# Kernel tuning notes

Measured on AMD Instinct MI355X. Metric: run time of the kernel, lower is better.

Reference implementation:

```python
import jax, jax.numpy as jnp
import numpy as np

C_M = 256
C_Z = 128
S = 256   # number of MSA sequences (global `s` in source)
R = 384   # number of residues (global `r` in source)
C = 32    # per-head channel dim
H = 8     # N_head
EPS = 1e-5


def _layer_norm(x, w, b):
    mu = jnp.mean(x, axis=-1, keepdims=True)
    var = jnp.mean(jnp.square(x - mu), axis=-1, keepdims=True)
    return (x - mu) * jax.lax.rsqrt(var + EPS) * w + b


def setup_inputs() -> dict:
    key = jax.random.key(0)
    ks = jax.random.split(key, 8)
    w = 0.02
    return {
        "msa": jax.random.normal(ks[0], (S, R, C_M), dtype=jnp.float32),
        "pair": jax.random.normal(ks[1], (R, R, C_Z), dtype=jnp.float32),
        "norm_msa_w": jnp.ones((H, C_M), jnp.float32),
        "norm_msa_b": jnp.zeros((H, C_M), jnp.float32),
        "wq": jax.random.normal(ks[2], (H, C, C_M), dtype=jnp.float32) * w,
        "wk": jax.random.normal(ks[3], (H, C, C_M), dtype=jnp.float32) * w,
        "wv": jax.random.normal(ks[4], (H, C, C_M), dtype=jnp.float32) * w,
        "norm_pair_w": jnp.ones((H, C_Z), jnp.float32),
        "norm_pair_b": jnp.zeros((H, C_Z), jnp.float32),
        "wb": jax.random.normal(ks[5], (H, S, C_Z), dtype=jnp.float32) * w,
        "wg": jax.random.normal(ks[6], (H, C, C_M), dtype=jnp.float32) * w,
        "out_w": jax.random.normal(ks[7], (C_M, C * H), dtype=jnp.float32) * w,
        "out_b": jnp.zeros((C_M,), jnp.float32),
    }


def reference(msa, pair, norm_msa_w, norm_msa_b, wq, wk, wv,
              norm_pair_w, norm_pair_b, wb, wg, out_w, out_b):
    inv_sqrt_c = 1.0 / np.sqrt(C).astype(np.float32)
    pair_flat = pair.reshape(-1, C_Z)  # (R*R, C_Z); view(-1, c_z)
    outs = []
    for i in range(H):
        # NOTE: faithful to source — msa is OVERWRITTEN by the per-head norm,
        # so normalization compounds across the head loop.
        msa = _layer_norm(msa, norm_msa_w[i], norm_msa_b[i])
        q = jnp.einsum('src,dc->srd', msa, wq[i])  # (S,R,C)
        k = jnp.einsum('src,dc->srd', msa, wk[i])
        v = jnp.einsum('src,dc->srd', msa, wv[i])
        # pair bias: LN -> Linear(c_z -> s) -> reshape (not transpose!) to (S,R,R)
        b = jnp.einsum('pc,sc->ps', _layer_norm(pair_flat, norm_pair_w[i], norm_pair_b[i]), wb[i])
        b = b.reshape(S, R, R)
        g = jax.nn.sigmoid(jnp.einsum('src,dc->srd', msa, wg[i]))  # (S,R,C)
        logits = inv_sqrt_c * (jnp.einsum('src,stc->srt', q, k) + b)  # (S,R,R)
        a = jax.nn.softmax(logits, axis=-2)  # softmax over QUERY axis, as in source
        o = g * jnp.einsum('srt,stc->src', a, v)  # (S,R,C)
        outs.append(o)
    out = jnp.concatenate(outs, axis=2)  # (S,R,C*H)
    return jnp.einsum('srk,mk->srm', out, out_w) + out_b  # (S,R,C_M)
```

## Files before the change

### kernel.cpp

```cpp
#include <hip/hip_runtime.h>

typedef unsigned short bf16_t;
typedef uint4  __attribute__((may_alias)) uint4_a;
typedef uint2  __attribute__((may_alias)) uint2_a;
typedef float4 __attribute__((may_alias)) float4_a;
typedef short bf16x8 __attribute__((ext_vector_type(8)));
typedef bf16x8 __attribute__((may_alias)) bf16x8_a;
typedef float f32x4 __attribute__((ext_vector_type(4)));

#define MFMA16(a, b, c) __builtin_amdgcn_mfma_f32_16x16x32_bf16((a), (b), (c), 0, 0, 0)

constexpr int kS  = 256;
constexpr int kR  = 384;
constexpr int kCM = 256;
constexpr int kCZ = 128;
constexpr int kC  = 32;
constexpr int kH  = 8;
constexpr int kP  = kR * kR;
constexpr int kM  = kS * kR;

#define EPSF 1e-5f
#define SCALEF 0.17677669529663687f

__device__ __forceinline__ float bf2f(bf16_t u) {
  return __uint_as_float(((unsigned int)u) << 16);
}
__device__ __forceinline__ bf16_t f2bf(float f) {
  unsigned int u = __float_as_uint(f);
  u += 0x7fffu + ((u >> 16) & 1u);
  return (bf16_t)(u >> 16);
}

__global__ __launch_bounds__(256) void k_pair_fused(const float* __restrict__ pair,
                                                    bf16_t* __restrict__ pair_bf,
                                                    float* __restrict__ mu,
                                                    float* __restrict__ rstd) {
  int row = blockIdx.x * 8 + (threadIdx.x >> 5);
  int l = threadIdx.x & 31;
  const float* src = pair + (size_t)row * kCZ + l * 4;
  float4_a x = *(const float4_a*)src;
  float s1 = x.x + x.y + x.z + x.w;
  float s2 = x.x * x.x + x.y * x.y + x.z * x.z + x.w * x.w;
#pragma unroll
  for (int off = 16; off > 0; off >>= 1) {
    s1 += __shfl_xor(s1, off);
    s2 += __shfl_xor(s2, off);
  }
  float m = s1 * (1.0f / kCZ);
  float v = s2 * (1.0f / kCZ) - m * m;
  float rs = rsqrtf(fmaxf(v, 0.0f) + EPSF);
  if (l == 0) {
    mu[row] = m;
    rstd[row] = rs;
  }
  uint2 u;
  u.x = (unsigned)f2bf(x.x) | ((unsigned)f2bf(x.y) << 16);
  u.y = (unsigned)f2bf(x.z) | ((unsigned)f2bf(x.w) << 16);
  *(uint2_a*)(pair_bf + (size_t)row * kCZ + l * 4) = u;
}

__global__ __launch_bounds__(256) void k_msa_ln(const float* __restrict__ src_f,
                                                const bf16_t* __restrict__ src_b,
                                                bf16_t* __restrict__ dst,
                                                const float* __restrict__ wall,
                                                const float* __restrict__ ball,
                                                int head, int first) {
  int row = blockIdx.x * 8 + (threadIdx.x >> 5);
  int l = threadIdx.x & 31;
  int c0 = l * 8;
  float x[8];
  if (first) {
    float4_a a = *(const float4_a*)(src_f + (size_t)row * kCM + c0);
    float4_a b = *(const float4_a*)(src_f + (size_t)row * kCM + c0 + 4);
    x[0] = a.x; x[1] = a.y; x[2] = a.z; x[3] = a.w;
    x[4] = b.x; x[5] = b.y; x[6] = b.z; x[7] = b.w;
  } else {
    union { bf16x8 v; bf16_t h[8]; } uu;
    uu.v = *(const bf16x8_a*)(src_b + (size_t)row * kCM + c0);
#pragma unroll
    for (int j = 0; j < 8; ++j) x[j] = bf2f(uu.h[j]);
  }
  float s1 = 0.f, s2 = 0.f;
#pragma unroll
  for (int j = 0; j < 8; ++j) {
    s1 += x[j];
    s2 += x[j] * x[j];
  }
#pragma unroll
  for (int off = 16; off > 0; off >>= 1) {
    s1 += __shfl_xor(s1, off);
    s2 += __shfl_xor(s2, off);
  }
  float m = s1 * (1.0f / kCM);
  float var = s2 * (1.0f / kCM) - m * m;
  float rs = rsqrtf(fmaxf(var, 0.0f) + EPSF);
  float4_a wa = *(const float4_a*)(wall + head * kCM + c0);
  float4_a wb4 = *(const float4_a*)(wall + head * kCM + c0 + 4);
  float4_a ba = *(const float4_a*)(ball + head * kCM + c0);
  float4_a bb4 = *(const float4_a*)(ball + head * kCM + c0 + 4);
  float wv[8] = {wa.x, wa.y, wa.z, wa.w, wb4.x, wb4.y, wb4.z, wb4.w};
  float bv[8] = {ba.x, ba.y, ba.z, ba.w, bb4.x, bb4.y, bb4.z, bb4.w};
  bf16_t h[8];
#pragma unroll
  for (int j = 0; j < 8; ++j) h[j] = f2bf((x[j] - m) * rs * wv[j] + bv[j]);
  uint4 u;
  u.x = (unsigned)h[0] | ((unsigned)h[1] << 16);
  u.y = (unsigned)h[2] | ((unsigned)h[3] << 16);
  u.z = (unsigned)h[4] | ((unsigned)h[5] << 16);
  u.w = (unsigned)h[6] | ((unsigned)h[7] << 16);
  *(uint4_a*)(dst + (size_t)row * kCM + c0) = u;
}

__global__ __launch_bounds__(256) void k_pack_wcat_all(const float* __restrict__ wq,
                                                       const float* __restrict__ wk,
                                                       const float* __restrict__ wv,
                                                       const float* __restrict__ wg,
                                                       bf16_t* __restrict__ Wcat) {
  int gid = blockIdx.x * 256 + threadIdx.x;
  int head = gid >> 15;
  int idx = gid & 32767;
  int j = idx >> 8;
  int c = idx & 255;
  const float* src = (j < 32) ? wq : (j < 64) ? wk : (j < 96) ? wv : wg;
  int d = j & 31;
  Wcat[gid] = f2bf(src[(head * kC + d) * kCM + c]);
}

__global__ __launch_bounds__(256) void k_pack_bias_all(const float* __restrict__ wb,
                                                       const float* __restrict__ npw,
                                                       const float* __restrict__ npb,
                                                       bf16_t* __restrict__ wbeff,
                                                       float* __restrict__ beta,
                                                       float* __restrict__ sw) {
  int head = blockIdx.x;
  int j = threadIdx.x;
  float sb = 0.f, ssw = 0.f;
  for (int c = 0; c < kCZ; ++c) {
    float w = wb[(head * kS + j) * kCZ + c];
    float e = w * npw[head * kCZ + c];
    wbeff[(size_t)head * kS * kCZ + j * kCZ + c] = f2bf(e);
    ssw += e;
    sb += w * npb[head * kCZ + c];
  }
  sw[head * kS + j] = ssw;
  beta[head * kS + j] = sb;
}

__global__ __launch_bounds__(256) void k_pack_outw(const float* __restrict__ in,
                                                   bf16_t* __restrict__ out) {
  int i = blockIdx.x * 256 + threadIdx.x;
  out[i] = f2bf(in[i]);
}

__global__ __launch_bounds__(256) void k_gemm_qkvg_mx(const bf16_t* __restrict__ A,
                                                      const bf16_t* __restrict__ B,
                                                      bf16_t* __restrict__ q,
                                                      bf16_t* __restrict__ k,
                                                      bf16_t* __restrict__ v,
                                                      bf16_t* __restrict__ g) {
  __shared__ bf16_t As[128 * 32];
  __shared__ bf16_t Bs[128 * 32];
  int m0 = blockIdx.x * 128;
  int tid = threadIdx.x;
  int w = tid >> 6, L = tid & 63, l15 = L & 15, q4 = L >> 4;
  int wm = w >> 1, wn = w & 1;
  f32x4 acc[4][4] = {};
  for (int k0 = 0; k0 < 256; k0 += 32) {
#pragma unroll
    for (int rep = 0; rep < 2; ++rep) {
      int idx = tid + rep * 256;
      int row = idx >> 2, sg = idx & 3;
      *(uint4_a*)&As[row * 32 + sg * 8] = *(const uint4_a*)(A + (size_t)(m0 + row) * 256 + k0 + sg * 8);
      *(uint4_a*)&Bs[row * 32 + sg * 8] = *(const uint4_a*)(B + (size_t)row * 256 + k0 + sg * 8);
    }
    __syncthreads();
    bf16x8 af[4], bfr[4];
#pragma unroll
    for (int mt = 0; mt < 4; ++mt) af[mt] = *(const bf16x8_a*)&As[(wm * 64 + mt * 16 + l15) * 32 + q4 * 8];
#pragma unroll
    for (int nt = 0; nt < 4; ++nt) bfr[nt] = *(const bf16x8_a*)&Bs[(wn * 64 + nt * 16 + l15) * 32 + q4 * 8];
#pragma unroll
    for (int mt = 0; mt < 4; ++mt)
#pragma unroll
      for (int nt = 0; nt < 4; ++nt) acc[mt][nt] = MFMA16(af[mt], bfr[nt], acc[mt][nt]);
    __syncthreads();
  }
#pragma unroll
  for (int mt = 0; mt < 4; ++mt)
#pragma unroll
    for (int nt = 0; nt < 4; ++nt) {
      int n = wn * 64 + nt * 16 + l15;
      int mat = n >> 5, d = n & 31;
      bf16_t* tgt = (mat == 0) ? q : (mat == 1) ? k : (mat == 2) ? v : g;
#pragma unroll
      for (int i = 0; i < 4; ++i) {
        int m = m0 + wm * 64 + mt * 16 + q4 * 4 + i;
        float val = acc[mt][nt][i];
        if (mat == 3) val = 1.0f / (1.0f + __expf(-val));
        tgt[(size_t)m * kC + d] = f2bf(val);
      }
    }
}

__global__ __launch_bounds__(256) void k_gemm_bias_mx(const bf16_t* __restrict__ A,
                                                      const bf16_t* __restrict__ B,
                                                      const float* __restrict__ mu,
                                                      const float* __restrict__ rstd,
                                                      const float* __restrict__ sw,
                                                      const float* __restrict__ beta,
                                                      bf16_t* __restrict__ Bm) {
  __shared__ bf16_t As[128 * 32];
  __shared__ bf16_t Bs[128 * 32];
  int m0 = blockIdx.x * 128;
  int n0 = blockIdx.y * 128;
  int tid = threadIdx.x;
  int w = tid >> 6, L = tid & 63, l15 = L & 15, q4 = L >> 4;
  int wm = w >> 1, wn = w & 1;
  f32x4 acc[4][4] = {};
  for (int k0 = 0; k0 < 128; k0 += 32) {
#pragma unroll
    for (int rep = 0; rep < 2; ++rep) {
      int idx = tid + rep * 256;
      int row = idx >> 2, sg = idx & 3;
      *(uint4_a*)&As[row * 32 + sg * 8] = *(const uint4_a*)(A + (size_t)(m0 + row) * 128 + k0 + sg * 8);
      *(uint4_a*)&Bs[row * 32 + sg * 8] = *(const uint4_a*)(B + (size_t)(n0 + row) * 128 + k0 + sg * 8);
    }
    __syncthreads();
    bf16x8 af[4], bfr[4];
#pragma unroll
    for (int mt = 0; mt < 4; ++mt) af[mt] = *(const bf16x8_a*)&As[(wm * 64 + mt * 16 + l15) * 32 + q4 * 8];
#pragma unroll
    for (int nt = 0; nt < 4; ++nt) bfr[nt] = *(const bf16x8_a*)&Bs[(wn * 64 + nt * 16 + l15) * 32 + q4 * 8];
#pragma unroll
    for (int mt = 0; mt < 4; ++mt)
#pragma unroll
      for (int nt = 0; nt < 4; ++nt) acc[mt][nt] = MFMA16(af[mt], bfr[nt], acc[mt][nt]);
    __syncthreads();
  }
#pragma unroll
  for (int mt = 0; mt < 4; ++mt)
#pragma unroll
    for (int i = 0; i < 4; ++i) {
      int m = m0 + wm * 64 + mt * 16 + q4 * 4 + i;
      float mp = mu[m], rp = rstd[m];
#pragma unroll
      for (int nt = 0; nt < 4; ++nt) {
        int n = n0 + wn * 64 + nt * 16 + l15;
        float val = rp * (acc[mt][nt][i] - mp * sw[n]) + beta[n];
        Bm[(size_t)m * kS + n] = f2bf(val);
      }
    }
}

__global__ __launch_bounds__(256) void k_logits(const bf16_t* __restrict__ q,
                                                const bf16_t* __restrict__ kmat,
                                                bf16_t* __restrict__ Bm) {
  int s = blockIdx.y;
  int t0 = blockIdx.x * 64;
  int tid = threadIdx.x;
  int w = tid >> 6, L = tid & 63, l15 = L & 15, q4 = L >> 4;
  __shared__ float red[4][64];
  __shared__ float msh[64], dish[64];
  bf16_t* bmS = Bm + (size_t)s * kP;
  f32x4 acc[6][4];
#pragma unroll
  for (int rt = 0; rt < 6; ++rt)
#pragma unroll
    for (int nt = 0; nt < 4; ++nt)
#pragma unroll
      for (int i = 0; i < 4; ++i) {
        int r = w * 96 + rt * 16 + q4 * 4 + i;
        int t = t0 + nt * 16 + l15;
        acc[rt][nt][i] = bf2f(bmS[(size_t)r * kR + t]);
      }
  const bf16_t* qs = q + (size_t)s * kR * kC;
  const bf16_t* ks = kmat + (size_t)s * kR * kC;
  bf16x8 bfr[4];
#pragma unroll
  for (int nt = 0; nt < 4; ++nt)
    bfr[nt] = *(const bf16x8_a*)(ks + (size_t)(t0 + nt * 16 + l15) * kC + q4 * 8);
#pragma unroll
  for (int rt = 0; rt < 6; ++rt) {
    bf16x8 af = *(const bf16x8_a*)(qs + (size_t)(w * 96 + rt * 16 + l15) * kC + q4 * 8);
#pragma unroll
    for (int nt = 0; nt < 4; ++nt) acc[rt][nt] = MFMA16(af, bfr[nt], acc[rt][nt]);
  }
#pragma unroll
  for (int rt = 0; rt < 6; ++rt)
#pragma unroll
    for (int nt = 0; nt < 4; ++nt) acc[rt][nt] *= SCALEF;
  float mx[4] = {-3.0e38f, -3.0e38f, -3.0e38f, -3.0e38f};
#pragma unroll
  for (int rt = 0; rt < 6; ++rt)
#pragma unroll
    for (int nt = 0; nt < 4; ++nt)
#pragma unroll
      for (int i = 0; i < 4; ++i) mx[nt] = fmaxf(mx[nt], acc[rt][nt][i]);
#pragma unroll
  for (int nt = 0; nt < 4; ++nt) {
    mx[nt] = fmaxf(mx[nt], __shfl_xor(mx[nt], 16));
    mx[nt] = fmaxf(mx[nt], __shfl_xor(mx[nt], 32));
  }
  if (L < 16) {
#pragma unroll
    for (int nt = 0; nt < 4; ++nt) red[w][nt * 16 + L] = mx[nt];
  }
  __syncthreads();
  if (tid < 64) {
    float m = fmaxf(fmaxf(red[0][tid], red[1][tid]), fmaxf(red[2][tid], red[3][tid]));
    msh[tid] = m;
  }
  __syncthreads();
  float mt_[4];
#pragma unroll
  for (int nt = 0; nt < 4; ++nt) mt_[nt] = msh[nt * 16 + l15];
  float sm[4] = {0.f, 0.f, 0.f, 0.f};
#pragma unroll
  for (int rt = 0; rt < 6; ++rt)
#pragma unroll
    for (int nt = 0; nt < 4; ++nt)
#pragma unroll
      for (int i = 0; i < 4; ++i) {
        float e = __expf(acc[rt][nt][i] - mt_[nt]);
        acc[rt][nt][i] = e;
        sm[nt] += e;
      }
#pragma unroll
  for (int nt = 0; nt < 4; ++nt) {
    sm[nt] += __shfl_xor(sm[nt], 16);
    sm[nt] += __shfl_xor(sm[nt], 32);
  }
  __syncthreads();
  if (L < 16) {
#pragma unroll
    for (int nt = 0; nt < 4; ++nt) red[w][nt * 16 + L] = sm[nt];
  }
  __syncthreads();
  if (tid < 64) {
    float d = red[0][tid] + red[1][tid] + red[2][tid] + red[3][tid];
    dish[tid] = 1.0f / d;
  }
  __syncthreads();
  float di[4];
#pragma unroll
  for (int nt = 0; nt < 4; ++nt) di[nt] = dish[nt * 16 + l15];
#pragma unroll
  for (int rt = 0; rt < 6; ++rt)
#pragma unroll
    for (int nt = 0; nt < 4; ++nt)
#pragma unroll
      for (int i = 0; i < 4; ++i) {
        int r = w * 96 + rt * 16 + q4 * 4 + i;
        int t = t0 + nt * 16 + l15;
        bmS[(size_t)r * kR + t] = f2bf(acc[rt][nt][i] * di[nt]);
      }
}

__global__ __launch_bounds__(256) void k_pv(const bf16_t* __restrict__ Am,
                                            const bf16_t* __restrict__ v,
                                            const bf16_t* __restrict__ g,
                                            float* __restrict__ o, int head) {
  int s = blockIdx.y;
  int r0 = blockIdx.x * 64;
  int tid = threadIdx.x;
  int w = tid >> 6, L = tid & 63, l15 = L & 15, q4 = L >> 4;
  __shared__ bf16_t vT[32 * 392];
#pragma unroll
  for (int rep = 0; rep < 6; ++rep) {
    int idx = tid + rep * 256;
    int t = idx >> 2, sg = idx & 3;
    union { uint4 u; bf16_t h[8]; } uu;
    uu.u = *(const uint4_a*)(v + (size_t)(s * kR + t) * kC + sg * 8);
#pragma unroll
    for (int j = 0; j < 8; ++j) vT[(sg * 8 + j) * 392 + t] = uu.h[j];
  }
  __syncthreads();
  const bf16_t* aS = Am + (size_t)s * kP + (size_t)(r0 + 16 * w + l15) * kR;
  f32x4 acc[2] = {};
#pragma unroll
  for (int kk = 0; kk < 12; ++kk) {
    bf16x8 af = *(const bf16x8_a*)(aS + kk * 32 + q4 * 8);
#pragma unroll
    for (int nt = 0; nt < 2; ++nt) {
      bf16x8 bfv = *(const bf16x8_a*)&vT[(nt * 16 + l15) * 392 + kk * 32 + q4 * 8];
      acc[nt] = MFMA16(af, bfv, acc[nt]);
    }
  }
#pragma unroll
  for (int nt = 0; nt < 2; ++nt)
#pragma unroll
    for (int i = 0; i < 4; ++i) {
      int r = r0 + 16 * w + q4 * 4 + i;
      int c = nt * 16 + l15;
      float val = acc[nt][i] * bf2f(g[(size_t)(s * kR + r) * kC + c]);
      o[(size_t)(s * kR + r) * kCM + head * kC + c] = val;
    }
}

__global__ __launch_bounds__(256) void k_gemm_final_mx(const float* __restrict__ OA,
                                                       const bf16_t* __restrict__ Bw,
                                                       const float* __restrict__ bias,
                                                       float* __restrict__ out) {
  __shared__ bf16_t As[2 * 64 * 32];
  __shared__ bf16_t Bs[256 * 32];
  int m0 = blockIdx.x * 64;
  int tid = threadIdx.x;
  int w = tid >> 6, L = tid & 63, l15 = L & 15, q4 = L >> 4;
  f32x4 acc[4][4] = {};
  for (int kc = 0; kc < 256; kc += 32) {
    {
      int row = tid >> 2, sg = tid & 3;
      const float* src = OA + (size_t)(m0 + row) * kCM + kc + sg * 8;
      float4_a f0 = *(const float4_a*)src;
      float4_a f1 = *(const float4_a*)(src + 4);
      float ff[8] = {f0.x, f0.y, f0.z, f0.w, f1.x, f1.y, f1.z, f1.w};
      uint4 uh, ul;
      bf16_t hi[8], lo[8];
#pragma unroll
      for (int j = 0; j < 8; ++j) {
        hi[j] = f2bf(ff[j]);
        lo[j] = f2bf(ff[j] - bf2f(hi[j]));
      }
      uh.x = (unsigned)hi[0] | ((unsigned)hi[1] << 16); uh.y = (unsigned)hi[2] | ((unsigned)hi[3] << 16);
      uh.z = (unsigned)hi[4] | ((unsigned)hi[5] << 16); uh.w = (unsigned)hi[6] | ((unsigned)hi[7] << 16);
      ul.x = (unsigned)lo[0] | ((unsigned)lo[1] << 16); ul.y = (unsigned)lo[2] | ((unsigned)lo[3] << 16);
      ul.z = (unsigned)lo[4] | ((unsigned)lo[5] << 16); ul.w = (unsigned)lo[6] | ((unsigned)lo[7] << 16);
      *(uint4_a*)&As[row * 32 + sg * 8] = uh;
      *(uint4_a*)&As[2048 + row * 32 + sg * 8] = ul;
    }
#pragma unroll
    for (int rep = 0; rep < 4; ++rep) {
      int idx = tid + rep * 256;
      int row = idx >> 2, sg = idx & 3;
      *(uint4_a*)&Bs[row * 32 + sg * 8] = *(const uint4_a*)(Bw + (size_t)row * kCM + kc + sg * 8);
    }
    __syncthreads();
    bf16x8 bfr[4];
#pragma unroll
    for (int nt = 0; nt < 4; ++nt) bfr[nt] = *(const bf16x8_a*)&Bs[(w * 64 + nt * 16 + l15) * 32 + q4 * 8];
#pragma unroll
    for (int half = 0; half < 2; ++half)
#pragma unroll
      for (int mt = 0; mt < 4; ++mt) {
        bf16x8 af = *(const bf16x8_a*)&As[half * 2048 + (mt * 16 + l15) * 32 + q4 * 8];
#pragma unroll
        for (int nt = 0; nt < 4; ++nt) acc[mt][nt] = MFMA16(af, bfr[nt], acc[mt][nt]);
      }
    __syncthreads();
  }
#pragma unroll
  for (int mt = 0; mt < 4; ++mt)
#pragma unroll
    for (int nt = 0; nt < 4; ++nt) {
      int n = w * 64 + nt * 16 + l15;
      float bn = bias[n];
#pragma unroll
      for (int i = 0; i < 4; ++i) {
        int m = m0 + mt * 16 + q4 * 4 + i;
        out[(size_t)m * kCM + n] = acc[mt][nt][i] + bn;
      }
    }
}

extern "C" void kernel_launch(void* const* d_in, const int* in_sizes, int n_in,
                              void* d_out, int out_size, void* d_ws, size_t ws_size,
                              hipStream_t stream) {
  (void)in_sizes; (void)n_in; (void)out_size; (void)ws_size;
  const float* msa_in = (const float*)d_in[0];
  const float* pair   = (const float*)d_in[1];
  const float* nmw    = (const float*)d_in[2];
  const float* nmb    = (const float*)d_in[3];
  const float* wq     = (const float*)d_in[4];
  const float* wk     = (const float*)d_in[5];
  const float* wv     = (const float*)d_in[6];
  const float* npw    = (const float*)d_in[7];
  const float* npb    = (const float*)d_in[8];
  const float* wb     = (const float*)d_in[9];
  const float* wg     = (const float*)d_in[10];
  const float* outw   = (const float*)d_in[11];
  const float* outb   = (const float*)d_in[12];
  float* out = (float*)d_out;

  char* ws = (char*)d_ws;
  size_t off = 0;
  bf16_t* msa_cur  = (bf16_t*)(ws + off); off += (size_t)kM * kCM * 2;
  bf16_t* pair_bf  = (bf16_t*)(ws + off); off += (size_t)kP * kCZ * 2;
  bf16_t* Bm       = (bf16_t*)(ws + off); off += (size_t)kP * kS * 2;
  bf16_t* qb       = (bf16_t*)(ws + off); off += (size_t)kM * kC * 2;
  bf16_t* kb       = (bf16_t*)(ws + off); off += (size_t)kM * kC * 2;
  bf16_t* vb       = (bf16_t*)(ws + off); off += (size_t)kM * kC * 2;
  bf16_t* gb       = (bf16_t*)(ws + off); off += (size_t)kM * kC * 2;
  float* mu_p      = (float*)(ws + off);  off += (size_t)kP * 4;
  float* rstd_p    = (float*)(ws + off);  off += (size_t)kP * 4;
  bf16_t* Wcat_all = (bf16_t*)(ws + off); off += (size_t)kH * 128 * 256 * 2;
  bf16_t* wbef_all = (bf16_t*)(ws + off); off += (size_t)kH * 256 * 128 * 2;
  bf16_t* outw_bf  = (bf16_t*)(ws + off); off += (size_t)256 * 256 * 2;
  float* beta_all  = (float*)(ws + off);  off += (size_t)kH * 256 * 4;
  float* sw_all    = (float*)(ws + off);  off += (size_t)kH * 256 * 4;

  k_pair_fused<<<kP / 8, 256, 0, stream>>>(pair, pair_bf, mu_p, rstd_p);
  k_pack_outw<<<256, 256, 0, stream>>>(outw, outw_bf);
  k_pack_wcat_all<<<kH * 128, 256, 0, stream>>>(wq, wk, wv, wg, Wcat_all);
  k_pack_bias_all<<<kH, 256, 0, stream>>>(wb, npw, npb, wbef_all, beta_all, sw_all);

  for (int h = 0; h < kH; ++h) {
    k_msa_ln<<<kM / 8, 256, 0, stream>>>(msa_in, msa_cur, msa_cur, nmw, nmb, h, h == 0 ? 1 : 0);
    k_gemm_qkvg_mx<<<kM / 128, 256, 0, stream>>>(msa_cur, Wcat_all + (size_t)h * 128 * 256,
                                                 qb, kb, vb, gb);
    k_gemm_bias_mx<<<dim3(kP / 128, 2), 256, 0, stream>>>(pair_bf, wbef_all + (size_t)h * 256 * 128,
                                                          mu_p, rstd_p,
                                                          sw_all + h * 256, beta_all + h * 256, Bm);
    k_logits<<<dim3(6, kS), 256, 0, stream>>>(qb, kb, Bm);
    k_pv<<<dim3(6, kS), 256, 0, stream>>>(Bm, vb, gb, out, h);
  }

  k_gemm_final_mx<<<kM / 64, 256, 0, stream>>>(out, outw_bf, outb, out);
}
```

Measured before the change: 1.513 ms.

## Fuse logits, softmax and PV into one attention kernel per head

After: 1.325 ms. 12.5% less time.

```diff
diff --git a/kernel.cpp b/kernel.cpp
--- a/kernel.cpp
+++ b/kernel.cpp
@@ -137,13 +137,13 @@
   float sb = 0.f, ssw = 0.f;
   for (int c = 0; c < kCZ; ++c) {
     float w = wb[(head * kS + j) * kCZ + c];
-    float e = w * npw[head * kCZ + c];
+    float e = w * npw[head * kCZ + c] * SCALEF;
     wbeff[(size_t)head * kS * kCZ + j * kCZ + c] = f2bf(e);
     ssw += e;
     sb += w * npb[head * kCZ + c];
   }
   sw[head * kS + j] = ssw;
-  beta[head * kS + j] = sb;
+  beta[head * kS + j] = sb * SCALEF;
 }
 
 __global__ __launch_bounds__(256) void k_pack_outw(const float* __restrict__ in,
@@ -157,7 +157,8 @@
                                                       bf16_t* __restrict__ q,
                                                       bf16_t* __restrict__ k,
                                                       bf16_t* __restrict__ v,
-                                                      bf16_t* __restrict__ g) {
+                                                      bf16_t* __restrict__ g_all,
+                                                      int head) {
   __shared__ bf16_t As[128 * 32];
   __shared__ bf16_t Bs[128 * 32];
   int m0 = blockIdx.x * 128;
@@ -191,13 +192,20 @@
     for (int nt = 0; nt < 4; ++nt) {
       int n = wn * 64 + nt * 16 + l15;
       int mat = n >> 5, d = n & 31;
-      bf16_t* tgt = (mat == 0) ? q : (mat == 1) ? k : (mat == 2) ? v : g;
 #pragma unroll
       for (int i = 0; i < 4; ++i) {
         int m = m0 + wm * 64 + mt * 16 + q4 * 4 + i;
         float val = acc[mt][nt][i];
-        if (mat == 3) val = 1.0f / (1.0f + __expf(-val));
-        tgt[(size_t)m * kC + d] = f2bf(val);
+        if (mat == 0) {
+          q[(size_t)m * kC + d] = f2bf(val * SCALEF);
+        } else if (mat == 1) {
+          k[(size_t)m * kC + d] = f2bf(val);
+        } else if (mat == 2) {
+          v[(size_t)m * kC + d] = f2bf(val);
+        } else {
+          float sg = 1.0f / (1.0f + __expf(-val));
+          g_all[(size_t)m * kCM + head * kC + d] = f2bf(sg);
+        }
       }
     }
 }
@@ -252,152 +260,132 @@
     }
 }
 
-__global__ __launch_bounds__(256) void k_logits(const bf16_t* __restrict__ q,
-                                                const bf16_t* __restrict__ kmat,
-                                                bf16_t* __restrict__ Bm) {
-  int s = blockIdx.y;
-  int t0 = blockIdx.x * 64;
+__global__ __launch_bounds__(256, 1) void k_attn(const bf16_t* __restrict__ q,
+                                                 const bf16_t* __restrict__ kmat,
+                                                 const bf16_t* __restrict__ v,
+                                                 const bf16_t* __restrict__ Bm,
+                                                 float* __restrict__ o0,
+                                                 float* __restrict__ o1,
+                                                 int head) {
+  int tb = blockIdx.x;
+  int s  = blockIdx.y;
   int tid = threadIdx.x;
   int w = tid >> 6, L = tid & 63, l15 = L & 15, q4 = L >> 4;
-  __shared__ float red[4][64];
-  __shared__ float msh[64], dish[64];
-  bf16_t* bmS = Bm + (size_t)s * kP;
-  f32x4 acc[6][4];
-#pragma unroll
-  for (int rt = 0; rt < 6; ++rt)
-#pragma unroll
-    for (int nt = 0; nt < 4; ++nt)
-#pragma unroll
-      for (int i = 0; i < 4; ++i) {
-        int r = w * 96 + rt * 16 + q4 * 4 + i;
-        int t = t0 + nt * 16 + l15;
-        acc[rt][nt][i] = bf2f(bmS[(size_t)r * kR + t]);
-      }
-  const bf16_t* qs = q + (size_t)s * kR * kC;
-  const bf16_t* ks = kmat + (size_t)s * kR * kC;
-  bf16x8 bfr[4];
-#pragma unroll
-  for (int nt = 0; nt < 4; ++nt)
-    bfr[nt] = *(const bf16x8_a*)(ks + (size_t)(t0 + nt * 16 + l15) * kC + q4 * 8);
-#pragma unroll
-  for (int rt = 0; rt < 6; ++rt) {
-    bf16x8 af = *(const bf16x8_a*)(qs + (size_t)(w * 96 + rt * 16 + l15) * kC + q4 * 8);
-#pragma unroll
-    for (int nt = 0; nt < 4; ++nt) acc[rt][nt] = MFMA16(af, bfr[nt], acc[rt][nt]);
-  }
-#pragma unroll
-  for (int rt = 0; rt < 6; ++rt)
-#pragma unroll
-    for (int nt = 0; nt < 4; ++nt) acc[rt][nt] *= SCALEF;
-  float mx[4] = {-3.0e38f, -3.0e38f, -3.0e38f, -3.0e38f};
-#pragma unroll
-  for (int rt = 0; rt < 6; ++rt)
-#pragma unroll
-    for (int nt = 0; nt < 4; ++nt)
-#pragma unroll
-      for (int i = 0; i < 4; ++i) mx[nt] = fmaxf(mx[nt], acc[rt][nt][i]);
-#pragma unroll
-  for (int nt = 0; nt < 4; ++nt) {
-    mx[nt] = fmaxf(mx[nt], __shfl_xor(mx[nt], 16));
-    mx[nt] = fmaxf(mx[nt], __shfl_xor(mx[nt], 32));
-  }
-  if (L < 16) {
-#pragma unroll
-    for (int nt = 0; nt < 4; ++nt) red[w][nt * 16 + L] = mx[nt];
-  }
-  __syncthreads();
-  if (tid < 64) {
-    float m = fmaxf(fmaxf(red[0][tid], red[1][tid]), fmaxf(red[2][tid], red[3][tid]));
-    msh[tid] = m;
-  }
-  __syncthreads();
-  float mt_[4];
-#pragma unroll
-  for (int nt = 0; nt < 4; ++nt) mt_[nt] = msh[nt * 16 + l15];
-  float sm[4] = {0.f, 0.f, 0.f, 0.f};
-#pragma unroll
-  for (int rt = 0; rt < 6; ++rt)
-#pragma unroll
-    for (int nt = 0; nt < 4; ++nt)
-#pragma unroll
-      for (int i = 0; i < 4; ++i) {
-        float e = __expf(acc[rt][nt][i] - mt_[nt]);
-        acc[rt][nt][i] = e;
-        sm[nt] += e;
-      }
-#pragma unroll
-  for (int nt = 0; nt < 4; ++nt) {
-    sm[nt] += __shfl_xor(sm[nt], 16);
-    sm[nt] += __shfl_xor(sm[nt], 32);
-  }
-  __syncthreads();
-  if (L < 16) {
-#pragma unroll
-    for (int nt = 0; nt < 4; ++nt) red[w][nt * 16 + L] = sm[nt];
-  }
-  __syncthreads();
-  if (tid < 64) {
-    float d = red[0][tid] + red[1][tid] + red[2][tid] + red[3][tid];
-    dish[tid] = 1.0f / d;
-  }
-  __syncthreads();
-  float di[4];
-#pragma unroll
-  for (int nt = 0; nt < 4; ++nt) di[nt] = dish[nt * 16 + l15];
-#pragma unroll
-  for (int rt = 0; rt < 6; ++rt)
-#pragma unroll
-    for (int nt = 0; nt < 4; ++nt)
-#pragma unroll
-      for (int i = 0; i < 4; ++i) {
-        int r = w * 96 + rt * 16 + q4 * 4 + i;
-        int t = t0 + nt * 16 + l15;
-        bmS[(size_t)r * kR + t] = f2bf(acc[rt][nt][i] * di[nt]);
-      }
-}
-
-__global__ __launch_bounds__(256) void k_pv(const bf16_t* __restrict__ Am,
-                                            const bf16_t* __restrict__ v,
-                                            const bf16_t* __restrict__ g,
-                                            float* __restrict__ o, int head) {
-  int s = blockIdx.y;
-  int r0 = blockIdx.x * 64;
-  int tid = threadIdx.x;
-  int w = tid >> 6, L = tid & 63, l15 = L & 15, q4 = L >> 4;
-  __shared__ bf16_t vT[32 * 392];
-#pragma unroll
-  for (int rep = 0; rep < 6; ++rep) {
+  float* opart = tb ? o1 : o0;
+  __shared__ bf16_t vT[32 * 200];
+  __shared__ bf16_t Psh[64 * 192];
+
+  int tbase = tb * 192;
+#pragma unroll
+  for (int rep = 0; rep < 3; ++rep) {
     int idx = tid + rep * 256;
     int t = idx >> 2, sg = idx & 3;
     union { uint4 u; bf16_t h[8]; } uu;
-    uu.u = *(const uint4_a*)(v + (size_t)(s * kR + t) * kC + sg * 8);
-#pragma unroll
-    for (int j = 0; j < 8; ++j) vT[(sg * 8 + j) * 392 + t] = uu.h[j];
+    uu.u = *(const uint4_a*)(v + (size_t)(s * kR + tbase + t) * kC + sg * 8);
+#pragma unroll
+    for (int j = 0; j < 8; ++j) vT[(sg * 8 + j) * 200 + t] = uu.h[j];
   }
   __syncthreads();
-  const bf16_t* aS = Am + (size_t)s * kP + (size_t)(r0 + 16 * w + l15) * kR;
-  f32x4 acc[2] = {};
-#pragma unroll
-  for (int kk = 0; kk < 12; ++kk) {
-    bf16x8 af = *(const bf16x8_a*)(aS + kk * 32 + q4 * 8);
-#pragma unroll
-    for (int nt = 0; nt < 2; ++nt) {
-      bf16x8 bfv = *(const bf16x8_a*)&vT[(nt * 16 + l15) * 392 + kk * 32 + q4 * 8];
-      acc[nt] = MFMA16(af, bfv, acc[nt]);
-    }
-  }
-#pragma unroll
-  for (int nt = 0; nt < 2; ++nt)
-#pragma unroll
-    for (int i = 0; i < 4; ++i) {
-      int r = r0 + 16 * w + q4 * 4 + i;
-      int c = nt * 16 + l15;
-      float val = acc[nt][i] * bf2f(g[(size_t)(s * kR + r) * kC + c]);
-      o[(size_t)(s * kR + r) * kCM + head * kC + c] = val;
-    }
-}
-
-__global__ __launch_bounds__(256) void k_gemm_final_mx(const float* __restrict__ OA,
+  bf16x8 bfv[12];
+#pragma unroll
+  for (int kk = 0; kk < 6; ++kk)
+#pragma unroll
+    for (int ct = 0; ct < 2; ++ct)
+      bfv[kk * 2 + ct] = *(const bf16x8_a*)&vT[(ct * 16 + l15) * 200 + kk * 32 + q4 * 8];
+
+  int t0 = tbase + 48 * w;
+  const bf16_t* bmS = Bm + (size_t)s * kP;
+  f32x4 acc[24][3];
+#pragma unroll
+  for (int rt = 0; rt < 24; ++rt)
+#pragma unroll
+    for (int tt = 0; tt < 3; ++tt)
+#pragma unroll
+      for (int i = 0; i < 4; ++i)
+        acc[rt][tt][i] = bf2f(bmS[(size_t)(rt * 16 + q4 * 4 + i) * kR + t0 + tt * 16 + l15]);
+
+  const bf16_t* qs = q + (size_t)s * kR * kC;
+  const bf16_t* kp = kmat + (size_t)s * kR * kC;
+  bf16x8 bk[3];
+#pragma unroll
+  for (int tt = 0; tt < 3; ++tt)
+    bk[tt] = *(const bf16x8_a*)(kp + (size_t)(t0 + tt * 16 + l15) * kC + q4 * 8);
+#pragma unroll
+  for (int rt = 0; rt < 24; ++rt) {
+    bf16x8 af = *(const bf16x8_a*)(qs + (size_t)(rt * 16 + l15) * kC + q4 * 8);
+#pragma unroll
+    for (int tt = 0; tt < 3; ++tt) acc[rt][tt] = MFMA16(af, bk[tt], acc[rt][tt]);
+  }
+
+  float mx[3] = {-3.0e38f, -3.0e38f, -3.0e38f};
+#pragma unroll
+  for (int rt = 0; rt < 24; ++rt)
+#pragma unroll
+    for (int tt = 0; tt < 3; ++tt)
+#pragma unroll
+      for (int i = 0; i < 4; ++i) mx[tt] = fmaxf(mx[tt], acc[rt][tt][i]);
+#pragma unroll
+  for (int tt = 0; tt < 3; ++tt) {
+    mx[tt] = fmaxf(mx[tt], __shfl_xor(mx[tt], 16));
+    mx[tt] = fmaxf(mx[tt], __shfl_xor(mx[tt], 32));
+  }
+  float sm[3] = {0.f, 0.f, 0.f};
+#pragma unroll
+  for (int rt = 0; rt < 24; ++rt)
+#pragma unroll
+    for (int tt = 0; tt < 3; ++tt)
+#pragma unroll
+      for (int i = 0; i < 4; ++i) {
+        float e = __expf(acc[rt][tt][i] - mx[tt]);
+        acc[rt][tt][i] = e;
+        sm[tt] += e;
+      }
+#pragma unroll
+  for (int tt = 0; tt < 3; ++tt) {
+    sm[tt] += __shfl_xor(sm[tt], 16);
+    sm[tt] += __shfl_xor(sm[tt], 32);
+  }
+  float di[3];
+#pragma unroll
+  for (int tt = 0; tt < 3; ++tt) di[tt] = 1.0f / sm[tt];
+
+#pragma unroll
+  for (int c = 0; c < 6; ++c) {
+#pragma unroll
+    for (int j = 0; j < 4; ++j)
+#pragma unroll
+      for (int tt = 0; tt < 3; ++tt)
+#pragma unroll
+        for (int i = 0; i < 4; ++i) {
+          int rl = j * 16 + q4 * 4 + i;
+          int tl = 48 * w + tt * 16 + l15;
+          Psh[rl * 192 + (tl ^ ((rl & 7) << 3))] = f2bf(acc[4 * c + j][tt][i] * di[tt]);
+        }
+    __syncthreads();
+    f32x4 pacc[2] = {};
+    int rr = w * 16 + l15;
+#pragma unroll
+    for (int kk = 0; kk < 6; ++kk) {
+      int e = kk * 32 + q4 * 8;
+      bf16x8 af = *(const bf16x8_a*)&Psh[rr * 192 + (e ^ ((rr & 7) << 3))];
+#pragma unroll
+      for (int ct = 0; ct < 2; ++ct) pacc[ct] = MFMA16(af, bfv[kk * 2 + ct], pacc[ct]);
+    }
+#pragma unroll
+    for (int ct = 0; ct < 2; ++ct)
+#pragma unroll
+      for (int i = 0; i < 4; ++i) {
+        int r = c * 64 + w * 16 + q4 * 4 + i;
+        int cc = ct * 16 + l15;
+        opart[(size_t)(s * kR + r) * kCM + head * kC + cc] = pacc[ct][i];
+      }
+    __syncthreads();
+  }
+}
+
+__global__ __launch_bounds__(256) void k_gemm_final_mx(const float* __restrict__ pA,
+                                                       const float* __restrict__ pB,
+                                                       const bf16_t* __restrict__ gall,
                                                        const bf16_t* __restrict__ Bw,
                                                        const float* __restrict__ bias,
                                                        float* __restrict__ out) {
@@ -410,10 +398,17 @@
   for (int kc = 0; kc < 256; kc += 32) {
     {
       int row = tid >> 2, sg = tid & 3;
-      const float* src = OA + (size_t)(m0 + row) * kCM + kc + sg * 8;
-      float4_a f0 = *(const float4_a*)src;
-      float4_a f1 = *(const float4_a*)(src + 4);
-      float ff[8] = {f0.x, f0.y, f0.z, f0.w, f1.x, f1.y, f1.z, f1.w};
+      size_t base = (size_t)(m0 + row) * kCM + kc + sg * 8;
+      float4_a a0 = *(const float4_a*)(pA + base);
+      float4_a a1 = *(const float4_a*)(pA + base + 4);
+      float4_a b0 = *(const float4_a*)(pB + base);
+      float4_a b1 = *(const float4_a*)(pB + base + 4);
+      union { bf16x8 v; bf16_t h[8]; } gg;
+      gg.v = *(const bf16x8_a*)(gall + base);
+      float ff[8] = {a0.x + b0.x, a0.y + b0.y, a0.z + b0.z, a0.w + b0.w,
+                     a1.x + b1.x, a1.y + b1.y, a1.z + b1.z, a1.w + b1.w};
+#pragma unroll
+      for (int j = 0; j < 8; ++j) ff[j] *= bf2f(gg.h[j]);
       uint4 uh, ul;
       bf16_t hi[8], lo[8];
 #pragma unroll
@@ -489,7 +484,8 @@
   bf16_t* qb       = (bf16_t*)(ws + off); off += (size_t)kM * kC * 2;
   bf16_t* kb       = (bf16_t*)(ws + off); off += (size_t)kM * kC * 2;
   bf16_t* vb       = (bf16_t*)(ws + off); off += (size_t)kM * kC * 2;
-  bf16_t* gb       = (bf16_t*)(ws + off); off += (size_t)kM * kC * 2;
+  bf16_t* g_all    = (bf16_t*)(ws + off); off += (size_t)kM * kCM * 2;
+  float*  pB       = (float*)(ws + off);  off += (size_t)kM * kCM * 4;
   float* mu_p      = (float*)(ws + off);  off += (size_t)kP * 4;
   float* rstd_p    = (float*)(ws + off);  off += (size_t)kP * 4;
   bf16_t* Wcat_all = (bf16_t*)(ws + off); off += (size_t)kH * 128 * 256 * 2;
@@ -506,13 +502,12 @@
   for (int h = 0; h < kH; ++h) {
     k_msa_ln<<<kM / 8, 256, 0, stream>>>(msa_in, msa_cur, msa_cur, nmw, nmb, h, h == 0 ? 1 : 0);
     k_gemm_qkvg_mx<<<kM / 128, 256, 0, stream>>>(msa_cur, Wcat_all + (size_t)h * 128 * 256,
-                                                 qb, kb, vb, gb);
+                                                 qb, kb, vb, g_all, h);
     k_gemm_bias_mx<<<dim3(kP / 128, 2), 256, 0, stream>>>(pair_bf, wbef_all + (size_t)h * 256 * 128,
                                                           mu_p, rstd_p,
                                                           sw_all + h * 256, beta_all + h * 256, Bm);
-    k_logits<<<dim3(6, kS), 256, 0, stream>>>(qb, kb, Bm);
-    k_pv<<<dim3(6, kS), 256, 0, stream>>>(Bm, vb, gb, out, h);
-  }
-
-  k_gemm_final_mx<<<kM / 64, 256, 0, stream>>>(out, outw_bf, outb, out);
-}
+    k_attn<<<dim3(2, kS), 256, 0, stream>>>(qb, kb, vb, Bm, out, pB, h);
+  }
+
+  k_gemm_final_mx<<<kM / 64, 256, 0, stream>>>(out, pB, g_all, outw_bf, outb, out);
+}
```
